# Kernel optimization log

Measured on AMD Instinct MI355X. Metric: run time of the kernel, lower is better.

Reference implementation:

```python
import jax, jax.numpy as jnp
import numpy as np

DIM = 4096
N_EXPERTS = 256
TOPK = 8
N_GROUPS = 8
TOPK_GROUPS = 4
ROUTE_SCALE = 2.5
N_TOKENS = 16384


def setup_inputs() -> dict:
    key = jax.random.key(0)
    k1, k2 = jax.random.split(key)
    x = jax.random.normal(k1, (N_TOKENS, DIM), dtype=jnp.float32)
    weight = jax.random.normal(k2, (N_EXPERTS, DIM), dtype=jnp.float32) * 0.01
    e_score_correction_bias = jnp.zeros((N_EXPERTS,), dtype=jnp.float32)
    return {"x": x, "weight": weight, "e_score_correction_bias": e_score_correction_bias}


def reference(x, weight, e_score_correction_bias):
    n = x.shape[0]
    # [n, E] expert scores
    scores = jax.nn.sigmoid(jnp.dot(x, weight.T))
    original_scores = scores
    scores = scores + e_score_correction_bias
    # group selection: top-2 sum per group -> top-k groups
    scores_g = scores.reshape(n, N_GROUPS, -1)  # [n, G, E/G]
    group_score = jnp.sort(scores_g, axis=-1)[..., -2:].sum(axis=-1)  # [n, G]
    group_idx = jnp.argsort(group_score, axis=-1)[..., -TOPK_GROUPS:]  # [n, kg]
    mask = jnp.ones((n, N_GROUPS), dtype=bool)
    mask = mask.at[jnp.arange(n)[:, None], group_idx].set(False)
    scores_masked = jnp.where(mask[..., None], -jnp.inf, scores_g).reshape(n, -1)
    # final top-k experts
    indices = jnp.argsort(scores_masked, axis=-1)[..., -TOPK:]  # [n, k]
    weights = original_scores[jnp.arange(n)[:, None], indices]  # [n, k]
    weights = weights / (weights.sum(axis=-1, keepdims=True) + 1e-20)
    weights = weights * ROUTE_SCALE
    return (weights, indices)
```

## Files before the change

kernel.cpp:

```cpp
#include <hip/hip_runtime.h>
#include <math.h>

#define DIMK 4096
#define NEXP 256
#define BM   64
#define BK32 32
#define NT   (DIMK / BK32)
#define NGRP 8
#define GSZ  32
#define TOPKG 4
#define TOPKE 8
#define WS_NEED ((size_t)NT * 3 * 16 * 1024)

#define LDSB_OFF 0
#define BTILE    49152
#define LDSX_OFF 98304
#define XTILE    12288
#define SMEM_SZ  131584

typedef __bf16 bf16x8 __attribute__((ext_vector_type(8)));
typedef float f32x4 __attribute__((ext_vector_type(4)));

__device__ __forceinline__ void gl16(const void* g, void* l) {
  __builtin_amdgcn_global_load_lds(
      (const __attribute__((address_space(1))) unsigned int*)g,
      (__attribute__((address_space(3))) unsigned int*)l, 16, 0, 0);
}

__device__ __forceinline__ void decomp8(const float v[8], uint4& H, uint4& M, uint4& L) {
  union U { __bf16 b[8]; uint4 u; } h, m, l;
#pragma unroll
  for (int i = 0; i < 8; ++i) {
    float xv = v[i];
    __bf16 hb = (__bf16)xv;
    float r1 = xv - (float)hb;
    __bf16 mb = (__bf16)r1;
    float r2 = r1 - (float)mb;
    h.b[i] = hb; m.b[i] = mb; l.b[i] = (__bf16)r2;
  }
  H = h.u; M = m.u; L = l.u;
}

__device__ __forceinline__ void decomp4(float4 v, uint2& H, uint2& M, uint2& L) {
  union U { __bf16 b[4]; uint2 u; } h, m, l;
  float vv[4] = {v.x, v.y, v.z, v.w};
#pragma unroll
  for (int i = 0; i < 4; ++i) {
    float xv = vv[i];
    __bf16 hb = (__bf16)xv;
    float r1 = xv - (float)hb;
    __bf16 mb = (__bf16)r1;
    float r2 = r1 - (float)mb;
    h.b[i] = hb; m.b[i] = mb; l.b[i] = (__bf16)r2;
  }
  H = h.u; M = m.u; L = l.u;
}

__global__ __launch_bounds__(256) void w_split_kernel(const float* __restrict__ wgt,
                                                      unsigned char* __restrict__ ws) {
  const int g = blockIdx.x * 256 + threadIdx.x;
  const int e = g >> 9;
  const int k0 = (g & 511) << 3;
  const int kt = k0 >> 5;
  const int chunk = (k0 & 31) >> 3;
  const int lane = chunk * 16 + (e & 15);
  const int eb = e >> 4;
  float v[8];
  float4 a = *(const float4*)(wgt + (long)e * DIMK + k0);
  float4 b = *(const float4*)(wgt + (long)e * DIMK + k0 + 4);
  v[0]=a.x; v[1]=a.y; v[2]=a.z; v[3]=a.w; v[4]=b.x; v[5]=b.y; v[6]=b.z; v[7]=b.w;
  uint4 H, M, L;
  decomp8(v, H, M, L);
  const long base = ((long)(kt * 3) * 16 + eb) * 1024 + lane * 16;
  *(uint4*)(ws + base)             = H;
  *(uint4*)(ws + base + 16 * 1024) = M;
  *(uint4*)(ws + base + 32 * 1024) = L;
}

__global__ __launch_bounds__(512) void moe_gate_mfma(
    const float* __restrict__ x, const unsigned char* __restrict__ ws,
    const float* __restrict__ bias, float* __restrict__ outw, float* __restrict__ outi) {
  __shared__ __align__(16) unsigned char smem[SMEM_SZ];
  double* sc = (double*)smem;

  const int tid = threadIdx.x;
  const int lane = tid & 63;
  const int l15 = lane & 15;
  const int wid = tid >> 6;
  const int wr = wid >> 2;
  const int wc = wid & 3;
  const long bm0 = (long)blockIdx.x * BM;

  const int xtok = tid >> 3;
  const int xq = tid & 7;
  const float* xptr = x + (bm0 + xtok) * (long)DIMK + xq * 4;
  const int xwoff = LDSX_OFF + (xq >> 1) * 1024 + xtok * 16 + (xq & 1) * 8;

  const unsigned char* wsp = ws + tid * 16;
  const int bldsw = LDSB_OFF + wid * 1024;

  f32x4 D[2][4];
  double acc[2][4][4];
#pragma unroll
  for (int rt = 0; rt < 2; ++rt)
#pragma unroll
    for (int ct = 0; ct < 4; ++ct) {
      D[rt][ct] = (f32x4){0.f, 0.f, 0.f, 0.f};
#pragma unroll
      for (int r = 0; r < 4; ++r) acc[rt][ct][r] = 0.0;
    }

  float4 xv;

#pragma unroll
  for (int j = 0; j < 6; ++j)
    gl16(wsp + j * 8192, smem + bldsw + j * 8192);
  xv = *(const float4*)(xptr);
  {
    uint2 H, M, L;
    decomp4(xv, H, M, L);
    *(uint2*)(smem + xwoff + 0 * 4096) = H;
    *(uint2*)(smem + xwoff + 1 * 4096) = M;
    *(uint2*)(smem + xwoff + 2 * 4096) = L;
  }
  __syncthreads();

#define MM(A, B, RT, CT) \
  D[RT][CT] = __builtin_amdgcn_mfma_f32_16x16x32_bf16(A, B, D[RT][CT], 0, 0, 0)
#define PASS2(A0, A1) \
  MM(A0, b0, 0, 0); MM(A0, b1, 0, 1); MM(A0, b2, 0, 2); MM(A0, b3, 0, 3); \
  MM(A1, b0, 1, 0); MM(A1, b1, 1, 1); MM(A1, b2, 1, 2); MM(A1, b3, 1, 3)

#pragma unroll 1
  for (int t = 0; t < NT; ++t) {
    const int buf = t & 1, nbuf = buf ^ 1;
    const bool more = (t + 1 < NT);
    if (more) {
      const unsigned char* wst = wsp + (long)(t + 1) * BTILE;
      const int bl = LDSB_OFF + nbuf * BTILE + wid * 1024;
#pragma unroll
      for (int j = 0; j < 6; ++j)
        gl16(wst + j * 8192, smem + bl + j * 8192);
      xv = *(const float4*)(xptr + (t + 1) * BK32);
    }
    const unsigned char* xb = smem + LDSX_OFF + buf * XTILE;
    const int ao0 = (lane >> 4) * 1024 + (wr * 32 + l15) * 16;
    const int ao1 = ao0 + 256;
    bf16x8 ah0 = *(const bf16x8*)(xb + 0 * 4096 + ao0);
    bf16x8 ah1 = *(const bf16x8*)(xb + 0 * 4096 + ao1);
    bf16x8 am0 = *(const bf16x8*)(xb + 1 * 4096 + ao0);
    bf16x8 am1 = *(const bf16x8*)(xb + 1 * 4096 + ao1);
    bf16x8 al0 = *(const bf16x8*)(xb + 2 * 4096 + ao0);
    bf16x8 al1 = *(const bf16x8*)(xb + 2 * 4096 + ao1);
    const unsigned char* bb = smem + LDSB_OFF + buf * BTILE + (wc * 4) * 1024 + lane * 16;
    bf16x8 b0, b1, b2, b3;
    __builtin_amdgcn_s_setprio(1);
    b0 = *(const bf16x8*)(bb + 0 * 16384 + 0 * 1024);
    b1 = *(const bf16x8*)(bb + 0 * 16384 + 1 * 1024);
    b2 = *(const bf16x8*)(bb + 0 * 16384 + 2 * 1024);
    b3 = *(const bf16x8*)(bb + 0 * 16384 + 3 * 1024);
    PASS2(ah0, ah1);
    PASS2(am0, am1);
    PASS2(al0, al1);
    b0 = *(const bf16x8*)(bb + 1 * 16384 + 0 * 1024);
    b1 = *(const bf16x8*)(bb + 1 * 16384 + 1 * 1024);
    b2 = *(const bf16x8*)(bb + 1 * 16384 + 2 * 1024);
    b3 = *(const bf16x8*)(bb + 1 * 16384 + 3 * 1024);
    PASS2(ah0, ah1);
    PASS2(am0, am1);
    b0 = *(const bf16x8*)(bb + 2 * 16384 + 0 * 1024);
    b1 = *(const bf16x8*)(bb + 2 * 16384 + 1 * 1024);
    b2 = *(const bf16x8*)(bb + 2 * 16384 + 2 * 1024);
    b3 = *(const bf16x8*)(bb + 2 * 16384 + 3 * 1024);
    PASS2(ah0, ah1);
    __builtin_amdgcn_s_setprio(0);
    if (more) {
      uint2 H, M, L;
      decomp4(xv, H, M, L);
      unsigned char* xw = smem + xwoff + nbuf * XTILE;
      *(uint2*)(xw + 0 * 4096) = H;
      *(uint2*)(xw + 1 * 4096) = M;
      *(uint2*)(xw + 2 * 4096) = L;
    }
    if (t & 1) {
#pragma unroll
      for (int rt = 0; rt < 2; ++rt)
#pragma unroll
        for (int ct = 0; ct < 4; ++ct) {
#pragma unroll
          for (int r = 0; r < 4; ++r) acc[rt][ct][r] += (double)D[rt][ct][r];
          D[rt][ct] = (f32x4){0.f, 0.f, 0.f, 0.f};
        }
    }
    __syncthreads();
  }
#undef PASS2
#undef MM

#pragma unroll
  for (int rt = 0; rt < 2; ++rt)
#pragma unroll
    for (int ct = 0; ct < 4; ++ct) {
      const int col = wc * 64 + ct * 16 + l15;
      const double bd = (double)bias[col];
#pragma unroll
      for (int r = 0; r < 4; ++r) {
        const int row = wr * 32 + rt * 16 + (lane >> 4) * 4 + r;
        const double s = 1.0 / (1.0 + exp(-acc[rt][ct][r]));
        sc[row * 257 + col] = s + bd;
      }
    }
  __syncthreads();

  if (tid < BM) {
    double* row = sc + tid * 257;
    double gs[NGRP];
#pragma unroll
    for (int g = 0; g < NGRP; ++g) {
      double m1 = -1e300, m2 = -1e300;
      for (int e = 0; e < GSZ; ++e) {
        double v = row[g * GSZ + e];
        if (v > m1) { m2 = m1; m1 = v; }
        else if (v > m2) { m2 = v; }
      }
      gs[g] = m1 + m2;
    }
    unsigned msk = 0;
#pragma unroll
    for (int g = 0; g < NGRP; ++g) {
      int cnt = 0;
#pragma unroll
      for (int h = 0; h < NGRP; ++h)
        cnt += ((gs[h] > gs[g]) || (gs[h] == gs[g] && h > g)) ? 1 : 0;
      if (cnt < TOPKG) msk |= (1u << g);
    }
    int g0 = __ffs(msk) - 1; msk &= msk - 1;
    int g1 = __ffs(msk) - 1; msk &= msk - 1;
    int g2 = __ffs(msk) - 1; msk &= msk - 1;
    int g3 = __ffs(msk) - 1;

    double wv[TOPKE];
    float iv[TOPKE];
#pragma unroll
    for (int r8 = 0; r8 < TOPKE; ++r8) {
      double best = -1e300;
      int bi = 0;
      {
        int gg = g0;
        for (int e = 0; e < GSZ; ++e) { double v = row[gg * GSZ + e]; if (v >= best) { best = v; bi = gg * GSZ + e; } }
        gg = g1;
        for (int e = 0; e < GSZ; ++e) { double v = row[gg * GSZ + e]; if (v >= best) { best = v; bi = gg * GSZ + e; } }
        gg = g2;
        for (int e = 0; e < GSZ; ++e) { double v = row[gg * GSZ + e]; if (v >= best) { best = v; bi = gg * GSZ + e; } }
        gg = g3;
        for (int e = 0; e < GSZ; ++e) { double v = row[gg * GSZ + e]; if (v >= best) { best = v; bi = gg * GSZ + e; } }
      }
      row[bi] = -1e300;
      wv[7 - r8] = best - (double)bias[bi];
      iv[7 - r8] = (float)bi;
    }
    double sum = 0.0;
#pragma unroll
    for (int p = 0; p < TOPKE; ++p) sum += wv[p];
    const double den = sum + 1e-20;
    const long trow = bm0 + tid;
#pragma unroll
    for (int p = 0; p < TOPKE; ++p) {
      outw[trow * 8 + p] = (float)(wv[p] / den * 2.5);
      outi[trow * 8 + p] = iv[p];
    }
  }
}

#define BMF  64
#define BKF 16
#define LXSF 68
__global__ __launch_bounds__(256, 1) void moe_gate_f64(
    const float* __restrict__ x, const float* __restrict__ wgt,
    const float* __restrict__ bias, float* __restrict__ outw,
    float* __restrict__ outi) {
  __shared__ __align__(16) unsigned char smem[64 * 257 * 8];
  float* lw = (float*)smem;
  float* lx = (float*)(smem + 32768);
  double* sc = (double*)smem;
  const int tid = threadIdx.x;
  const long bm0 = (long)blockIdx.x * BMF;
  const int rg = tid >> 5;
  const int cg = tid & 31;
  const int sxr = tid >> 2;
  const int sxj = (tid & 3) << 2;
  const float* xrow = x + (bm0 + sxr) * (long)DIMK + sxj;
  const float* wrow = wgt + (long)tid * DIMK;
  double acc[8][8];
#pragma unroll
  for (int i = 0; i < 8; ++i)
#pragma unroll
    for (int j = 0; j < 8; ++j) acc[i][j] = 0.0;
#define LWF(b, k, e) lw[((b)*BKF + (k)) * NEXP + (e)]
#define LXF(b, k, r) lx[((b)*BKF + (k)) * LXSF + (r)]
  {
    float4 xv = *(const float4*)(xrow);
#pragma unroll
    for (int c = 0; c < 4; ++c) LXF(0, sxj + c, sxr) = ((const float*)&xv)[c];
#pragma unroll
    for (int jj = 0; jj < 4; ++jj) {
      float4 wv = *(const float4*)(wrow + jj * 4);
#pragma unroll
      for (int c = 0; c < 4; ++c) LWF(0, jj * 4 + c, tid) = ((const float*)&wv)[c];
    }
  }
  __syncthreads();
  const int NTF = DIMK / BKF;
  for (int kt = 0; kt < NTF; ++kt) {
    const int b = kt & 1;
    if (kt + 1 < NTF) {
      const int k0 = (kt + 1) * BKF;
      const int nb = b ^ 1;
      float4 xv = *(const float4*)(xrow + k0);
      float4 wv0 = *(const float4*)(wrow + k0);
      float4 wv1 = *(const float4*)(wrow + k0 + 4);
      float4 wv2 = *(const float4*)(wrow + k0 + 8);
      float4 wv3 = *(const float4*)(wrow + k0 + 12);
#pragma unroll
      for (int c = 0; c < 4; ++c) LXF(nb, sxj + c, sxr) = ((const float*)&xv)[c];
#pragma unroll
      for (int c = 0; c < 4; ++c) LWF(nb, 0 + c, tid) = ((const float*)&wv0)[c];
#pragma unroll
      for (int c = 0; c < 4; ++c) LWF(nb, 4 + c, tid) = ((const float*)&wv1)[c];
#pragma unroll
      for (int c = 0; c < 4; ++c) LWF(nb, 8 + c, tid) = ((const float*)&wv2)[c];
#pragma unroll
      for (int c = 0; c < 4; ++c) LWF(nb, 12 + c, tid) = ((const float*)&wv3)[c];
    }
#pragma unroll
    for (int k = 0; k < BKF; ++k) {
      float4 a0 = *(const float4*)(&LXF(b, k, rg * 8));
      float4 a1 = *(const float4*)(&LXF(b, k, rg * 8 + 4));
      double ad[8] = {(double)a0.x, (double)a0.y, (double)a0.z, (double)a0.w,
                      (double)a1.x, (double)a1.y, (double)a1.z, (double)a1.w};
      double bd[8];
#pragma unroll
      for (int j = 0; j < 4; ++j) {
        float2 bb = *(const float2*)(&LWF(b, k, cg * 2 + 64 * j));
        bd[2 * j] = (double)bb.x;
        bd[2 * j + 1] = (double)bb.y;
      }
#pragma unroll
      for (int i = 0; i < 8; ++i)
#pragma unroll
        for (int j = 0; j < 8; ++j) acc[i][j] += ad[i] * bd[j];
    }
    __syncthreads();
  }
  double bc[8];
#pragma unroll
  for (int j = 0; j < 4; ++j) {
    bc[2 * j] = (double)bias[cg * 2 + 64 * j];
    bc[2 * j + 1] = (double)bias[cg * 2 + 64 * j + 1];
  }
#pragma unroll
  for (int i = 0; i < 8; ++i) {
    const int r = rg * 8 + i;
#pragma unroll
    for (int jq = 0; jq < 8; ++jq) {
      const int col = cg * 2 + 64 * (jq >> 1) + (jq & 1);
      double s = 1.0 / (1.0 + exp(-acc[i][jq]));
      sc[r * 257 + col] = s + bc[jq];
    }
  }
  __syncthreads();
  if (tid < BMF) {
    double* row = sc + tid * 257;
    double gs[NGRP];
#pragma unroll
    for (int g = 0; g < NGRP; ++g) {
      double m1 = -1e300, m2 = -1e300;
      for (int e = 0; e < GSZ; ++e) {
        double v = row[g * GSZ + e];
        if (v > m1) { m2 = m1; m1 = v; }
        else if (v > m2) { m2 = v; }
      }
      gs[g] = m1 + m2;
    }
    unsigned msk = 0;
#pragma unroll
    for (int g = 0; g < NGRP; ++g) {
      int cnt = 0;
#pragma unroll
      for (int h = 0; h < NGRP; ++h)
        cnt += ((gs[h] > gs[g]) || (gs[h] == gs[g] && h > g)) ? 1 : 0;
      if (cnt < TOPKG) msk |= (1u << g);
    }
    int g0 = __ffs(msk) - 1; msk &= msk - 1;
    int g1 = __ffs(msk) - 1; msk &= msk - 1;
    int g2 = __ffs(msk) - 1; msk &= msk - 1;
    int g3 = __ffs(msk) - 1;
    double wv[TOPKE];
    float iv[TOPKE];
#pragma unroll
    for (int r8 = 0; r8 < TOPKE; ++r8) {
      double best = -1e300;
      int bi = 0;
      {
        int gg = g0;
        for (int e = 0; e < GSZ; ++e) { double v = row[gg * GSZ + e]; if (v >= best) { best = v; bi = gg * GSZ + e; } }
        gg = g1;
        for (int e = 0; e < GSZ; ++e) { double v = row[gg * GSZ + e]; if (v >= best) { best = v; bi = gg * GSZ + e; } }
        gg = g2;
        for (int e = 0; e < GSZ; ++e) { double v = row[gg * GSZ + e]; if (v >= best) { best = v; bi = gg * GSZ + e; } }
        gg = g3;
        for (int e = 0; e < GSZ; ++e) { double v = row[gg * GSZ + e]; if (v >= best) { best = v; bi = gg * GSZ + e; } }
      }
      row[bi] = -1e300;
      wv[7 - r8] = best - (double)bias[bi];
      iv[7 - r8] = (float)bi;
    }
    double sum = 0.0;
#pragma unroll
    for (int p = 0; p < TOPKE; ++p) sum += wv[p];
    const double den = sum + 1e-20;
    const long trow = bm0 + tid;
#pragma unroll
    for (int p = 0; p < TOPKE; ++p) {
      outw[trow * 8 + p] = (float)(wv[p] / den * 2.5);
      outi[trow * 8 + p] = iv[p];
    }
  }
}

extern "C" void kernel_launch(void* const* d_in, const int* in_sizes, int n_in,
                              void* d_out, int out_size, void* d_ws, size_t ws_size,
                              hipStream_t stream) {
  const float* x = (const float*)d_in[0];
  const float* w = (const float*)d_in[1];
  const float* b = (const float*)d_in[2];
  const int ntok = in_sizes[0] / DIMK;
  float* outw = (float*)d_out;
  float* outi = outw + (size_t)ntok * 8;
  if (ws_size >= WS_NEED) {
    hipLaunchKernelGGL(w_split_kernel, dim3(512), dim3(256), 0, stream,
                       w, (unsigned char*)d_ws);
    hipLaunchKernelGGL(moe_gate_mfma, dim3(ntok / BM), dim3(512), 0, stream,
                       x, (const unsigned char*)d_ws, b, outw, outi);
  } else {
    hipLaunchKernelGGL(moe_gate_f64, dim3(ntok / 64), dim3(256), 0, stream,
                       x, w, b, outw, outi);
  }
}
```

Before: 232.9 us.

## Load weight fragments directly from global into registers instead of staging via LDS

Replaces the LDS double-buffered staging of the pre-split bf16 weight tiles (global_load_lds) with direct per-lane global loads into registers, prefetching the next k-tile's fragments right after each fragment's last use. This removes the LDS write/read traffic for B. The cost is that each of the two row-waves loads the same B fragments from global/L2 (duplicate traffic), it holds 12 extra vector registers per lane, and it relies on per-iteration global latency being hidden by the MFMA work.

New measurement: 228.6 us. About the same (-1.8%).

```diff
diff --git a/kernel.cpp b/kernel.cpp
--- a/kernel.cpp
+++ b/kernel.cpp
@@ -10,22 +10,14 @@
 #define GSZ  32
 #define TOPKG 4
 #define TOPKE 8
-#define WS_NEED ((size_t)NT * 3 * 16 * 1024)
-
-#define LDSB_OFF 0
-#define BTILE    49152
-#define LDSX_OFF 98304
-#define XTILE    12288
-#define SMEM_SZ  131584
+#define BTILE 49152
+#define WS_NEED ((size_t)NT * BTILE)
+
+#define XTILE   12288
+#define SMEM_SZ 131584
 
 typedef __bf16 bf16x8 __attribute__((ext_vector_type(8)));
 typedef float f32x4 __attribute__((ext_vector_type(4)));
-
-__device__ __forceinline__ void gl16(const void* g, void* l) {
-  __builtin_amdgcn_global_load_lds(
-      (const __attribute__((address_space(1))) unsigned int*)g,
-      (__attribute__((address_space(3))) unsigned int*)l, 16, 0, 0);
-}
 
 __device__ __forceinline__ void decomp8(const float v[8], uint4& H, uint4& M, uint4& L) {
   union U { __bf16 b[8]; uint4 u; } h, m, l;
@@ -94,10 +86,9 @@
   const int xtok = tid >> 3;
   const int xq = tid & 7;
   const float* xptr = x + (bm0 + xtok) * (long)DIMK + xq * 4;
-  const int xwoff = LDSX_OFF + (xq >> 1) * 1024 + xtok * 16 + (xq & 1) * 8;
-
-  const unsigned char* wsp = ws + tid * 16;
-  const int bldsw = LDSB_OFF + wid * 1024;
+  const int xwoff = (xq >> 1) * 1024 + xtok * 16 + (xq & 1) * 8;
+
+  const unsigned char* wsb = ws + (wc * 4) * 1024 + lane * 16;
 
   f32x4 D[2][4];
   double acc[2][4][4];
@@ -111,10 +102,20 @@
     }
 
   float4 xv;
-
-#pragma unroll
-  for (int j = 0; j < 6; ++j)
-    gl16(wsp + j * 8192, smem + bldsw + j * 8192);
+  bf16x8 bh0, bh1, bh2, bh3, bm0r, bm1r, bm2r, bm3r, bl0, bl1, bl2, bl3;
+
+  bh0 = *(const bf16x8*)(wsb + 0 * 16384 + 0 * 1024);
+  bh1 = *(const bf16x8*)(wsb + 0 * 16384 + 1 * 1024);
+  bh2 = *(const bf16x8*)(wsb + 0 * 16384 + 2 * 1024);
+  bh3 = *(const bf16x8*)(wsb + 0 * 16384 + 3 * 1024);
+  bm0r = *(const bf16x8*)(wsb + 1 * 16384 + 0 * 1024);
+  bm1r = *(const bf16x8*)(wsb + 1 * 16384 + 1 * 1024);
+  bm2r = *(const bf16x8*)(wsb + 1 * 16384 + 2 * 1024);
+  bm3r = *(const bf16x8*)(wsb + 1 * 16384 + 3 * 1024);
+  bl0 = *(const bf16x8*)(wsb + 2 * 16384 + 0 * 1024);
+  bl1 = *(const bf16x8*)(wsb + 2 * 16384 + 1 * 1024);
+  bl2 = *(const bf16x8*)(wsb + 2 * 16384 + 2 * 1024);
+  bl3 = *(const bf16x8*)(wsb + 2 * 16384 + 3 * 1024);
   xv = *(const float4*)(xptr);
   {
     uint2 H, M, L;
@@ -127,23 +128,18 @@
 
 #define MM(A, B, RT, CT) \
   D[RT][CT] = __builtin_amdgcn_mfma_f32_16x16x32_bf16(A, B, D[RT][CT], 0, 0, 0)
-#define PASS2(A0, A1) \
-  MM(A0, b0, 0, 0); MM(A0, b1, 0, 1); MM(A0, b2, 0, 2); MM(A0, b3, 0, 3); \
-  MM(A1, b0, 1, 0); MM(A1, b1, 1, 1); MM(A1, b2, 1, 2); MM(A1, b3, 1, 3)
+#define P8(A0, A1, B0, B1, B2, B3) \
+  MM(A0, B0, 0, 0); MM(A0, B1, 0, 1); MM(A0, B2, 0, 2); MM(A0, B3, 0, 3); \
+  MM(A1, B0, 1, 0); MM(A1, B1, 1, 1); MM(A1, B2, 1, 2); MM(A1, B3, 1, 3)
+
+  long bo_n = BTILE;
 
 #pragma unroll 1
   for (int t = 0; t < NT; ++t) {
     const int buf = t & 1, nbuf = buf ^ 1;
     const bool more = (t + 1 < NT);
-    if (more) {
-      const unsigned char* wst = wsp + (long)(t + 1) * BTILE;
-      const int bl = LDSB_OFF + nbuf * BTILE + wid * 1024;
-#pragma unroll
-      for (int j = 0; j < 6; ++j)
-        gl16(wst + j * 8192, smem + bl + j * 8192);
-      xv = *(const float4*)(xptr + (t + 1) * BK32);
-    }
-    const unsigned char* xb = smem + LDSX_OFF + buf * XTILE;
+    if (more) xv = *(const float4*)(xptr + (t + 1) * BK32);
+    const unsigned char* xb = smem + buf * XTILE;
     const int ao0 = (lane >> 4) * 1024 + (wr * 32 + l15) * 16;
     const int ao1 = ao0 + 256;
     bf16x8 ah0 = *(const bf16x8*)(xb + 0 * 4096 + ao0);
@@ -152,32 +148,30 @@
     bf16x8 am1 = *(const bf16x8*)(xb + 1 * 4096 + ao1);
     bf16x8 al0 = *(const bf16x8*)(xb + 2 * 4096 + ao0);
     bf16x8 al1 = *(const bf16x8*)(xb + 2 * 4096 + ao1);
-    const unsigned char* bb = smem + LDSB_OFF + buf * BTILE + (wc * 4) * 1024 + lane * 16;
-    bf16x8 b0, b1, b2, b3;
     __builtin_amdgcn_s_setprio(1);
-    b0 = *(const bf16x8*)(bb + 0 * 16384 + 0 * 1024);
-    b1 = *(const bf16x8*)(bb + 0 * 16384 + 1 * 1024);
-    b2 = *(const bf16x8*)(bb + 0 * 16384 + 2 * 1024);
-    b3 = *(const bf16x8*)(bb + 0 * 16384 + 3 * 1024);
-    PASS2(ah0, ah1);
-    PASS2(am0, am1);
-    PASS2(al0, al1);
-    b0 = *(const bf16x8*)(bb + 1 * 16384 + 0 * 1024);
-    b1 = *(const bf16x8*)(bb + 1 * 16384 + 1 * 1024);
-    b2 = *(const bf16x8*)(bb + 1 * 16384 + 2 * 1024);
-    b3 = *(const bf16x8*)(bb + 1 * 16384 + 3 * 1024);
-    PASS2(ah0, ah1);
-    PASS2(am0, am1);
-    b0 = *(const bf16x8*)(bb + 2 * 16384 + 0 * 1024);
-    b1 = *(const bf16x8*)(bb + 2 * 16384 + 1 * 1024);
-    b2 = *(const bf16x8*)(bb + 2 * 16384 + 2 * 1024);
-    b3 = *(const bf16x8*)(bb + 2 * 16384 + 3 * 1024);
-    PASS2(ah0, ah1);
+    P8(ah0, ah1, bh0, bh1, bh2, bh3);
+    P8(am0, am1, bh0, bh1, bh2, bh3);
+    P8(al0, al1, bh0, bh1, bh2, bh3);
+    bh0 = *(const bf16x8*)(wsb + bo_n + 0 * 16384 + 0 * 1024);
+    bh1 = *(const bf16x8*)(wsb + bo_n + 0 * 16384 + 1 * 1024);
+    bh2 = *(const bf16x8*)(wsb + bo_n + 0 * 16384 + 2 * 1024);
+    bh3 = *(const bf16x8*)(wsb + bo_n + 0 * 16384 + 3 * 1024);
+    P8(ah0, ah1, bm0r, bm1r, bm2r, bm3r);
+    P8(am0, am1, bm0r, bm1r, bm2r, bm3r);
+    bm0r = *(const bf16x8*)(wsb + bo_n + 1 * 16384 + 0 * 1024);
+    bm1r = *(const bf16x8*)(wsb + bo_n + 1 * 16384 + 1 * 1024);
+    bm2r = *(const bf16x8*)(wsb + bo_n + 1 * 16384 + 2 * 1024);
+    bm3r = *(const bf16x8*)(wsb + bo_n + 1 * 16384 + 3 * 1024);
+    P8(ah0, ah1, bl0, bl1, bl2, bl3);
+    bl0 = *(const bf16x8*)(wsb + bo_n + 2 * 16384 + 0 * 1024);
+    bl1 = *(const bf16x8*)(wsb + bo_n + 2 * 16384 + 1 * 1024);
+    bl2 = *(const bf16x8*)(wsb + bo_n + 2 * 16384 + 2 * 1024);
+    bl3 = *(const bf16x8*)(wsb + bo_n + 2 * 16384 + 3 * 1024);
     __builtin_amdgcn_s_setprio(0);
     if (more) {
       uint2 H, M, L;
       decomp4(xv, H, M, L);
-      unsigned char* xw = smem + xwoff + nbuf * XTILE;
+      unsigned char* xw = smem + nbuf * XTILE + xwoff;
       *(uint2*)(xw + 0 * 4096) = H;
       *(uint2*)(xw + 1 * 4096) = M;
       *(uint2*)(xw + 2 * 4096) = L;
@@ -193,8 +187,9 @@
         }
     }
     __syncthreads();
-  }
-#undef PASS2
+    if (t + 2 < NT) bo_n += BTILE;
+  }
+#undef P8
 #undef MM
 
 #pragma unroll
```
